# Kernel optimization log

Hardware: AMD Instinct MI355X
Metric: run time of the kernel (lower is better)

Reference implementation:

```python
import jax, jax.numpy as jnp
import numpy as np

B = 65536       # batch size
C = 100         # num classes (len(cls_num_list))
ALPHA = 0.01    # soft-label blend weight
TAU = 2.0       # init arg tau
TEMP = 2.0      # distillation temperature
EPS = 1e-9


def _soft_ce(logits, soft_targets):
    # -(soft * log softmax(logits)).sum(1).mean()
    return -(soft_targets * jax.nn.log_softmax(logits, axis=1)).sum(axis=1).mean()


def _inverse_prior(prior):
    idx0 = jnp.argsort(prior)            # ascending sort permutation
    value = prior[idx0]                  # sorted values
    idx1 = jnp.argsort(idx0)             # rank of each element
    idx2 = prior.shape[0] - 1 - idx1     # mirrored rank
    return value[idx2]


def setup_inputs():
    key = jax.random.key(0)
    ks = jax.random.split(key, 8)
    cls_num = np.arange(500, 0, -5).astype(np.float32)  # matches init cls_num_list
    prior = jnp.asarray(cls_num / cls_num.sum(), dtype=jnp.float32)
    return {
        "output_logits": jax.random.normal(ks[0], (B, C), jnp.float32),
        "target": jax.random.randint(ks[1], (B,), 0, C),
        "cos_feature": jax.random.normal(ks[2], (C, C), jnp.float32),
        "old_pred": jax.random.normal(ks[3], (B, C), jnp.float32),
        "expert1_logits": jax.random.normal(ks[4], (B, C), jnp.float32),
        "expert2_logits": jax.random.normal(ks[5], (B, C), jnp.float32),
        "expert3_logits": jax.random.normal(ks[6], (B, C), jnp.float32),
        "output": jax.random.normal(ks[7], (B, C), jnp.float32),
        "prior": prior,
        "epoch": 5,
    }


def reference(output_logits, target, cos_feature, old_pred, expert1_logits,
              expert2_logits, expert3_logits, output, prior, epoch):
    num_classes = prior.shape[0]
    # ---- convert_to_soft_labels (vectorized: gather rows of sim matrix, softmax, blend) ----
    one_hot = jax.nn.one_hot(target, num_classes, dtype=jnp.float32)          # [B,C]
    sim_probs = jax.nn.softmax(cos_feature, axis=1)[target]                   # [B,C]
    label = (1.0 - ALPHA) * one_hot + ALPHA * sim_probs

    # ---- three expert soft cross-entropies ----
    log_prior = jnp.log(prior + EPS)
    loss = _soft_ce(expert1_logits, label)
    loss = loss + _soft_ce(expert2_logits + log_prior, label)
    inv_prior = _inverse_prior(prior)
    loss = loss + _soft_ce(expert3_logits + log_prior - TAU * jnp.log(inv_prior + EPS), label)

    # ---- bincount-normalized summed logits ----
    counts = jnp.bincount(target, length=num_classes).astype(jnp.float32)     # [C]
    num = counts[target][:, None]                                             # [B,1]
    expert_sum_logits = output / num                                          # [B,C]

    # ---- masked KL distillation (only rows where teacher argmax == target) ----
    teacher_index = jnp.argmax(old_pred, axis=1)                              # argmax(softmax)=argmax
    mask = (teacher_index == target).astype(jnp.float32)                      # [B]
    t = jax.nn.softmax(old_pred / TEMP, axis=1)                               # teacher probs
    s = jax.nn.log_softmax(expert_sum_logits / TEMP, axis=1)                  # student log-probs
    log_t = jnp.where(t > 0, jnp.log(t), 0.0)
    kl_per = (t * (log_t - s)).sum(axis=1)                                    # [B] per-row KL
    n_sel = mask.sum()
    kl_loss = jnp.where(n_sel > 0, (kl_per * mask).sum() / jnp.maximum(n_sel, 1.0), 0.0)
    kl_loss = kl_loss * (TEMP ** 2) * 3.0

    return loss, kl_loss, expert_sum_logits
```

## Files before the change

### kernel.cpp

```cpp
#include <hip/hip_runtime.h>
#include <math.h>

#define B_N 65536
#define C_N 100
constexpr float ALPHA = 0.01f;
constexpr float TAU   = 2.0f;
constexpr float TEMP  = 2.0f;
constexpr float EPSF  = 1e-9f;
constexpr float NEG_SENT = -1.0e30f;

template<int CTRL>
__device__ __forceinline__ float fadd_dpp(float x) {
    return x + __int_as_float(__builtin_amdgcn_update_dpp(
        0, __float_as_int(x), CTRL, 0xF, 0xF, true));
}
__device__ __forceinline__ float rowsum32(float x) {
    x = fadd_dpp<0xB1>(x);
    x = fadd_dpp<0x4E>(x);
    x = fadd_dpp<0x124>(x);
    x = fadd_dpp<0x128>(x);
    x = fadd_dpp<0x142>(x);
    return x;
}
template<int CTRL>
__device__ __forceinline__ void amax_dpp(unsigned &hi, unsigned &lo) {
    const unsigned yh = (unsigned)__builtin_amdgcn_update_dpp(0, (int)hi, CTRL, 0xF, 0xF, true);
    const unsigned yl = (unsigned)__builtin_amdgcn_update_dpp(0, (int)lo, CTRL, 0xF, 0xF, true);
    const bool take = (yh > hi) || (yh == hi && yl > lo);
    hi = take ? yh : hi;
    lo = take ? yl : lo;
}
__device__ __forceinline__ void rowamax32(unsigned &hi, unsigned &lo) {
    amax_dpp<0xB1>(hi, lo);
    amax_dpp<0x4E>(hi, lo);
    amax_dpp<0x124>(hi, lo);
    amax_dpp<0x128>(hi, lo);
    amax_dpp<0x142>(hi, lo);
}

__device__ __forceinline__ float wsum(float v) {
    #pragma unroll
    for (int o = 32; o; o >>= 1) v += __shfl_xor(v, o);
    return v;
}

__global__ void prep_k(const float* __restrict__ cosf, const float* __restrict__ prior,
                       const int* __restrict__ target,
                       float* __restrict__ sm, float* __restrict__ w2,
                       float* __restrict__ w3, float* __restrict__ Ht,
                       int* __restrict__ counts) {
    const int b = blockIdx.x;
    if (b < 256) {
        __shared__ int h[C_N];
        for (int i = threadIdx.x; i < C_N; i += blockDim.x) h[i] = 0;
        __syncthreads();
        const int gid = b * blockDim.x + threadIdx.x;
        const int stride = 256 * blockDim.x;
        for (int i = gid; i < B_N; i += stride) atomicAdd(&h[target[i]], 1);
        __syncthreads();
        for (int i = threadIdx.x; i < C_N; i += blockDim.x)
            if (h[i]) atomicAdd(&counts[i], h[i]);
    } else if (b == 256) {
        __shared__ float sp[C_N];
        __shared__ float val[C_N];
        const int t = threadIdx.x;
        if (t < C_N) sp[t] = prior[t];
        __syncthreads();
        int rank = 0;
        float lpi = 0.f, pi = 0.f;
        if (t < C_N) {
            pi = sp[t];
            for (int j = 0; j < C_N; ++j) {
                const float pj = sp[j];
                rank += (pj < pi) || (pj == pi && j < t);
            }
            val[rank] = pi;
            lpi = __logf(pi + EPSF);
        }
        __syncthreads();
        if (t < C_N) {
            const float inv = val[C_N - 1 - rank];
            const float c3v = lpi - TAU * __logf(inv + EPSF);
            w2[t] = pi + EPSF;
            w3[t] = __expf(c3v);
            Ht[t] = lpi + c3v;
        }
    } else {
        const int gw = (b - 257) * 4 + (threadIdx.x >> 6);
        const int lane = threadIdx.x & 63;
        for (int row = gw; row < C_N; row += 16) {
            const float* rp = cosf + row * C_N;
            const float v0 = rp[lane];
            const bool has1 = (lane + 64) < C_N;
            const float v1 = has1 ? rp[lane + 64] : -INFINITY;
            float m = fmaxf(v0, v1);
            #pragma unroll
            for (int o = 32; o; o >>= 1) m = fmaxf(m, __shfl_xor(m, o));
            const float e0 = __expf(v0 - m);
            const float e1 = has1 ? __expf(v1 - m) : 0.f;
            const float s = wsum(e0 + e1);
            const float is = 1.0f / s;
            sm[row * C_N + lane] = e0 * is;
            if (has1) sm[row * C_N + lane + 64] = e1 * is;
        }
    }
}

#define HBLK 4096
#define NBLK (2 * HBLK)

__launch_bounds__(256)
__global__ void main_k(const int* __restrict__ target,
                       const float* __restrict__ e1p, const float* __restrict__ e2p,
                       const float* __restrict__ e3p, const float* __restrict__ opp,
                       const float* __restrict__ outp,
                       const float* __restrict__ sm, const float* __restrict__ w2p,
                       const float* __restrict__ w3p, const float* __restrict__ Hp,
                       const int* __restrict__ counts,
                       float* __restrict__ dout,
                       float* __restrict__ ploss, float* __restrict__ pkl, float* __restrict__ pn) {
    const int lane = threadIdx.x & 63;
    const int gl   = lane & 31;
    const int half = lane >> 5;
    const int wslot = threadIdx.x >> 6;
    const bool act = gl < 25;
    const int c0 = 4 * gl;
    const bool own = (gl == 16);
    __shared__ float bl[4], bk[4], bn[4];

    if (blockIdx.x < HBLK) {
        const int gw = blockIdx.x * 4 + wslot;
        const int rowA = 4 * gw + half;
        const int rowB = 4 * gw + 2 + half;
        const int tgtA = target[rowA];
        const int tgtB = target[rowB];
        const int baseA = rowA * C_N;
        const int baseB = rowB * C_N;

        float4 W2 = make_float4(0,0,0,0), W3 = make_float4(0,0,0,0), HH = make_float4(0,0,0,0);
        float4 E1A, E2A, E3A, E1B, E2B, E3B, SMA, SMB;
        E1A = E2A = E3A = E1B = E2B = E3B = make_float4(NEG_SENT, NEG_SENT, NEG_SENT, NEG_SENT);
        SMA = SMB = make_float4(0,0,0,0);
        if (act) {
            W2  = *(const float4*)(w2p + c0);
            W3  = *(const float4*)(w3p + c0);
            HH  = *(const float4*)(Hp + c0);
            E1A = *(const float4*)(e1p + baseA + c0);
            E1B = *(const float4*)(e1p + baseB + c0);
            E2A = *(const float4*)(e2p + baseA + c0);
            E2B = *(const float4*)(e2p + baseB + c0);
            E3A = *(const float4*)(e3p + baseA + c0);
            E3B = *(const float4*)(e3p + baseB + c0);
            SMA = *(const float4*)(sm + tgtA * C_N + c0);
            SMB = *(const float4*)(sm + tgtB * C_N + c0);
        }

        const float laA0 = (1.0f - ALPHA) * (c0     == tgtA) + ALPHA * SMA.x;
        const float laA1 = (1.0f - ALPHA) * (c0 + 1 == tgtA) + ALPHA * SMA.y;
        const float laA2 = (1.0f - ALPHA) * (c0 + 2 == tgtA) + ALPHA * SMA.z;
        const float laA3 = (1.0f - ALPHA) * (c0 + 3 == tgtA) + ALPHA * SMA.w;
        float s1A = __expf(E1A.x) + __expf(E1A.y) + __expf(E1A.z) + __expf(E1A.w);
        float s2A = W2.x * __expf(E2A.x) + W2.y * __expf(E2A.y)
                  + W2.z * __expf(E2A.z) + W2.w * __expf(E2A.w);
        float s3A = W3.x * __expf(E3A.x) + W3.y * __expf(E3A.y)
                  + W3.z * __expf(E3A.z) + W3.w * __expf(E3A.w);
        float dtA = laA0 * (E1A.x + E2A.x + E3A.x + HH.x)
                  + laA1 * (E1A.y + E2A.y + E3A.y + HH.y)
                  + laA2 * (E1A.z + E2A.z + E3A.z + HH.z)
                  + laA3 * (E1A.w + E2A.w + E3A.w + HH.w);
        const float laB0 = (1.0f - ALPHA) * (c0     == tgtB) + ALPHA * SMB.x;
        const float laB1 = (1.0f - ALPHA) * (c0 + 1 == tgtB) + ALPHA * SMB.y;
        const float laB2 = (1.0f - ALPHA) * (c0 + 2 == tgtB) + ALPHA * SMB.z;
        const float laB3 = (1.0f - ALPHA) * (c0 + 3 == tgtB) + ALPHA * SMB.w;
        float s1B = __expf(E1B.x) + __expf(E1B.y) + __expf(E1B.z) + __expf(E1B.w);
        float s2B = W2.x * __expf(E2B.x) + W2.y * __expf(E2B.y)
                  + W2.z * __expf(E2B.z) + W2.w * __expf(E2B.w);
        float s3B = W3.x * __expf(E3B.x) + W3.y * __expf(E3B.y)
                  + W3.z * __expf(E3B.z) + W3.w * __expf(E3B.w);
        float dtB = laB0 * (E1B.x + E2B.x + E3B.x + HH.x)
                  + laB1 * (E1B.y + E2B.y + E3B.y + HH.y)
                  + laB2 * (E1B.z + E2B.z + E3B.z + HH.z)
                  + laB3 * (E1B.w + E2B.w + E3B.w + HH.w);

        s1A = rowsum32(s1A);  s1B = rowsum32(s1B);
        s2A = rowsum32(s2A);  s2B = rowsum32(s2B);
        s3A = rowsum32(s3A);  s3B = rowsum32(s3B);
        dtA = rowsum32(dtA);  dtB = rowsum32(dtB);

        const float ceA = __logf(s1A * s2A * s3A) - dtA;
        const float ceB = __logf(s1B * s2B * s3B) - dtB;
        float lossAcc = own ? (ceA + ceB) : 0.f;
        const float lossW = __shfl(lossAcc, 16) + __shfl(lossAcc, 48);
        if (lane == 0) bl[wslot] = lossW;
        __syncthreads();
        if (threadIdx.x == 0)
            ploss[blockIdx.x] = bl[0] + bl[1] + bl[2] + bl[3];
    } else {
        const int j  = blockIdx.x - HBLK;
        const int gw = j * 4 + wslot;
        const int rowA = 4 * gw + half;
        const int rowB = 4 * gw + 2 + half;
        const int tgtA = target[rowA];
        const int tgtB = target[rowB];
        const int baseA = rowA * C_N;
        const int baseB = rowB * C_N;

        float4 OPA, OUA, OPB, OUB;
        OPA = OUA = OPB = OUB = make_float4(NEG_SENT, NEG_SENT, NEG_SENT, NEG_SENT);
        if (act) {
            OPA = *(const float4*)(opp + baseA + c0);
            OPB = *(const float4*)(opp + baseB + c0);
            OUA = *(const float4*)(outp + baseA + c0);
            OUB = *(const float4*)(outp + baseB + c0);
        }
        const float rcA = 1.0f / (float)counts[tgtA];
        const float rcB = 1.0f / (float)counts[tgtB];

        const float aA0 = OPA.x * 0.5f, aA1 = OPA.y * 0.5f, aA2 = OPA.z * 0.5f, aA3 = OPA.w * 0.5f;
        const float pA0 = __expf(aA0), pA1 = __expf(aA1), pA2 = __expf(aA2), pA3 = __expf(aA3);
        float ztA = pA0 + pA1 + pA2 + pA3;
        float bvA = OPA.x; int biA = c0;
        if (OPA.y > bvA) { bvA = OPA.y; biA = c0 + 1; }
        if (OPA.z > bvA) { bvA = OPA.z; biA = c0 + 2; }
        if (OPA.w > bvA) { bvA = OPA.w; biA = c0 + 3; }
        unsigned bbA = __float_as_uint(bvA);
        bbA = ((int)bbA < 0) ? ~bbA : (bbA | 0x80000000u);
        unsigned khiA = bbA, kloA = (unsigned)~biA;
        const float esA0 = OUA.x * rcA, esA1 = OUA.y * rcA, esA2 = OUA.z * rcA, esA3 = OUA.w * rcA;
        const float xA0 = esA0 * 0.5f, xA1 = esA1 * 0.5f, xA2 = esA2 * 0.5f, xA3 = esA3 * 0.5f;
        float zsA = __expf(xA0) + __expf(xA1) + __expf(xA2) + __expf(xA3);
        float DA  = pA0 * (aA0 - xA0) + pA1 * (aA1 - xA1) + pA2 * (aA2 - xA2) + pA3 * (aA3 - xA3);
        if (act) {
            *(float2*)(dout + 2 + baseA + c0)     = make_float2(esA0, esA1);
            *(float2*)(dout + 2 + baseA + c0 + 2) = make_float2(esA2, esA3);
        }
        const float aB0 = OPB.x * 0.5f, aB1 = OPB.y * 0.5f, aB2 = OPB.z * 0.5f, aB3 = OPB.w * 0.5f;
        const float pB0 = __expf(aB0), pB1 = __expf(aB1), pB2 = __expf(aB2), pB3 = __expf(aB3);
        float ztB = pB0 + pB1 + pB2 + pB3;
        float bvB = OPB.x; int biB = c0;
        if (OPB.y > bvB) { bvB = OPB.y; biB = c0 + 1; }
        if (OPB.z > bvB) { bvB = OPB.z; biB = c0 + 2; }
        if (OPB.w > bvB) { bvB = OPB.w; biB = c0 + 3; }
        unsigned bbB = __float_as_uint(bvB);
        bbB = ((int)bbB < 0) ? ~bbB : (bbB | 0x80000000u);
        unsigned khiB = bbB, kloB = (unsigned)~biB;
        const float esB0 = OUB.x * rcB, esB1 = OUB.y * rcB, esB2 = OUB.z * rcB, esB3 = OUB.w * rcB;
        const float xB0 = esB0 * 0.5f, xB1 = esB1 * 0.5f, xB2 = esB2 * 0.5f, xB3 = esB3 * 0.5f;
        float zsB = __expf(xB0) + __expf(xB1) + __expf(xB2) + __expf(xB3);
        float DB  = pB0 * (aB0 - xB0) + pB1 * (aB1 - xB1) + pB2 * (aB2 - xB2) + pB3 * (aB3 - xB3);
        if (act) {
            *(float2*)(dout + 2 + baseB + c0)     = make_float2(esB0, esB1);
            *(float2*)(dout + 2 + baseB + c0 + 2) = make_float2(esB2, esB3);
        }

        ztA = rowsum32(ztA);  ztB = rowsum32(ztB);
        zsA = rowsum32(zsA);  zsB = rowsum32(zsB);
        DA  = rowsum32(DA);   DB  = rowsum32(DB);
        rowamax32(khiA, kloA);
        rowamax32(khiB, kloB);

        const int miA = (int)~kloA;
        const int miB = (int)~kloB;
        const float rztA = 1.0f / ztA, rztB = 1.0f / ztB;
        const float klvA = DA * rztA + __logf(zsA * rztA);
        const float klvB = DB * rztB + __logf(zsB * rztB);
        const bool selA = own && (miA == tgtA);
        const bool selB = own && (miB == tgtB);
        float klAcc = (selA ? klvA : 0.f) + (selB ? klvB : 0.f);
        float nAcc  = (selA ? 1.f : 0.f) + (selB ? 1.f : 0.f);
        const float klW = __shfl(klAcc, 16) + __shfl(klAcc, 48);
        const float nW  = __shfl(nAcc, 16) + __shfl(nAcc, 48);
        if (lane == 0) { bk[wslot] = klW; bn[wslot] = nW; }
        __syncthreads();
        if (threadIdx.x == 0) {
            pkl[j] = bk[0] + bk[1] + bk[2] + bk[3];
            pn[j]  = bn[0] + bn[1] + bn[2] + bn[3];
        }
    }
}

__global__ void final_k(const float* __restrict__ ploss, const float* __restrict__ pkl,
                        const float* __restrict__ pn, float* __restrict__ dout) {
    __shared__ float sl[256], sk[256], sn[256];
    const int t = threadIdx.x;
    float l = 0.f, k = 0.f, n = 0.f;
    for (int i = t; i < HBLK; i += 256) { l += ploss[i]; k += pkl[i]; n += pn[i]; }
    sl[t] = l; sk[t] = k; sn[t] = n;
    __syncthreads();
    for (int s = 128; s; s >>= 1) {
        if (t < s) { sl[t] += sl[t + s]; sk[t] += sk[t + s]; sn[t] += sn[t + s]; }
        __syncthreads();
    }
    if (t == 0) {
        dout[0] = sl[0] / (float)B_N;
        const float kl = (sn[0] > 0.f) ? (sk[0] / fmaxf(sn[0], 1.f)) : 0.f;
        dout[1] = kl * (TEMP * TEMP) * 3.0f;
    }
}

extern "C" void kernel_launch(void* const* d_in, const int* in_sizes, int n_in,
                              void* d_out, int out_size, void* d_ws, size_t ws_size,
                              hipStream_t stream) {
    const int*   target = (const int*)  d_in[1];
    const float* cosf   = (const float*)d_in[2];
    const float* oldp   = (const float*)d_in[3];
    const float* e1     = (const float*)d_in[4];
    const float* e2     = (const float*)d_in[5];
    const float* e3     = (const float*)d_in[6];
    const float* outp   = (const float*)d_in[7];
    const float* prior  = (const float*)d_in[8];

    float* ws    = (float*)d_ws;
    float* sm    = ws;
    float* w2    = ws + 10016;
    float* w3    = ws + 10120;
    float* Ht    = ws + 10224;
    int*   cnts  = (int*)(ws + 10328);
    float* ploss = ws + 10432;
    float* pkl   = ploss + HBLK;
    float* pn    = pkl + HBLK;

    hipMemsetAsync(cnts, 0, C_N * sizeof(int), stream);
    prep_k<<<261, 256, 0, stream>>>(cosf, prior, target, sm, w2, w3, Ht, cnts);
    main_k<<<NBLK, 256, 0, stream>>>(target, e1, e2, e3, oldp, outp,
                                     sm, w2, w3, Ht, cnts, (float*)d_out, ploss, pkl, pn);
    final_k<<<1, 256, 0, stream>>>(ploss, pkl, pn, (float*)d_out);
}
```

Baseline: 51.79 us.

## Interleave block roles, use nontemporal output stores, and atomic bucketed partials

Even and odd blocks now alternate between the cross-entropy and KL roles, so both kinds of work run together across the GPU. The large normalized-logits output is written with nontemporal stores to avoid polluting cache. Per-block partials are accumulated into 256 buckets with float atomics, which shrinks the final reduction kernel. Occupancy is hinted via launch bounds. Float atomics make the summation order nondeterministic.

```diff
diff --git a/kernel.cpp b/kernel.cpp
--- a/kernel.cpp
+++ b/kernel.cpp
@@ -8,6 +8,8 @@
 constexpr float TEMP  = 2.0f;
 constexpr float EPSF  = 1e-9f;
 constexpr float NEG_SENT = -1.0e30f;
+
+typedef float v2f __attribute__((ext_vector_type(2)));
 
 template<int CTRL>
 __device__ __forceinline__ float fadd_dpp(float x) {
@@ -109,7 +111,7 @@
 #define HBLK 4096
 #define NBLK (2 * HBLK)
 
-__launch_bounds__(256)
+__launch_bounds__(256, 8)
 __global__ void main_k(const int* __restrict__ target,
                        const float* __restrict__ e1p, const float* __restrict__ e2p,
                        const float* __restrict__ e3p, const float* __restrict__ opp,
@@ -118,7 +120,7 @@
                        const float* __restrict__ w3p, const float* __restrict__ Hp,
                        const int* __restrict__ counts,
                        float* __restrict__ dout,
-                       float* __restrict__ ploss, float* __restrict__ pkl, float* __restrict__ pn) {
+                       float* __restrict__ pl, float* __restrict__ pk, float* __restrict__ pn) {
     const int lane = threadIdx.x & 63;
     const int gl   = lane & 31;
     const int half = lane >> 5;
@@ -127,9 +129,12 @@
     const int c0 = 4 * gl;
     const bool own = (gl == 16);
     __shared__ float bl[4], bk[4], bn[4];
-
-    if (blockIdx.x < HBLK) {
-        const int gw = blockIdx.x * 4 + wslot;
+    const int role = blockIdx.x & 1;
+    const int j    = blockIdx.x >> 1;
+    const int bucket = blockIdx.x & 255;
+
+    if (role == 0) {
+        const int gw = j * 4 + wslot;
         const int rowA = 4 * gw + half;
         const int rowB = 4 * gw + 2 + half;
         const int tgtA = target[rowA];
@@ -194,9 +199,8 @@
         if (lane == 0) bl[wslot] = lossW;
         __syncthreads();
         if (threadIdx.x == 0)
-            ploss[blockIdx.x] = bl[0] + bl[1] + bl[2] + bl[3];
+            atomicAdd(&pl[bucket], bl[0] + bl[1] + bl[2] + bl[3]);
     } else {
-        const int j  = blockIdx.x - HBLK;
         const int gw = j * 4 + wslot;
         const int rowA = 4 * gw + half;
         const int rowB = 4 * gw + 2 + half;
@@ -231,8 +235,10 @@
         float zsA = __expf(xA0) + __expf(xA1) + __expf(xA2) + __expf(xA3);
         float DA  = pA0 * (aA0 - xA0) + pA1 * (aA1 - xA1) + pA2 * (aA2 - xA2) + pA3 * (aA3 - xA3);
         if (act) {
-            *(float2*)(dout + 2 + baseA + c0)     = make_float2(esA0, esA1);
-            *(float2*)(dout + 2 + baseA + c0 + 2) = make_float2(esA2, esA3);
+            v2f w0 = { esA0, esA1 };
+            v2f w1 = { esA2, esA3 };
+            __builtin_nontemporal_store(w0, (v2f*)(dout + 2 + baseA + c0));
+            __builtin_nontemporal_store(w1, (v2f*)(dout + 2 + baseA + c0 + 2));
         }
         const float aB0 = OPB.x * 0.5f, aB1 = OPB.y * 0.5f, aB2 = OPB.z * 0.5f, aB3 = OPB.w * 0.5f;
         const float pB0 = __expf(aB0), pB1 = __expf(aB1), pB2 = __expf(aB2), pB3 = __expf(aB3);
@@ -249,8 +255,10 @@
         float zsB = __expf(xB0) + __expf(xB1) + __expf(xB2) + __expf(xB3);
         float DB  = pB0 * (aB0 - xB0) + pB1 * (aB1 - xB1) + pB2 * (aB2 - xB2) + pB3 * (aB3 - xB3);
         if (act) {
-            *(float2*)(dout + 2 + baseB + c0)     = make_float2(esB0, esB1);
-            *(float2*)(dout + 2 + baseB + c0 + 2) = make_float2(esB2, esB3);
+            v2f w0 = { esB0, esB1 };
+            v2f w1 = { esB2, esB3 };
+            __builtin_nontemporal_store(w0, (v2f*)(dout + 2 + baseB + c0));
+            __builtin_nontemporal_store(w1, (v2f*)(dout + 2 + baseB + c0 + 2));
         }
 
         ztA = rowsum32(ztA);  ztB = rowsum32(ztB);
@@ -273,19 +281,17 @@
         if (lane == 0) { bk[wslot] = klW; bn[wslot] = nW; }
         __syncthreads();
         if (threadIdx.x == 0) {
-            pkl[j] = bk[0] + bk[1] + bk[2] + bk[3];
-            pn[j]  = bn[0] + bn[1] + bn[2] + bn[3];
+            atomicAdd(&pk[bucket], bk[0] + bk[1] + bk[2] + bk[3]);
+            atomicAdd(&pn[bucket], bn[0] + bn[1] + bn[2] + bn[3]);
         }
     }
 }
 
-__global__ void final_k(const float* __restrict__ ploss, const float* __restrict__ pkl,
+__global__ void final_k(const float* __restrict__ pl, const float* __restrict__ pk,
                         const float* __restrict__ pn, float* __restrict__ dout) {
     __shared__ float sl[256], sk[256], sn[256];
     const int t = threadIdx.x;
-    float l = 0.f, k = 0.f, n = 0.f;
-    for (int i = t; i < HBLK; i += 256) { l += ploss[i]; k += pkl[i]; n += pn[i]; }
-    sl[t] = l; sk[t] = k; sn[t] = n;
+    sl[t] = pl[t]; sk[t] = pk[t]; sn[t] = pn[t];
     __syncthreads();
     for (int s = 128; s; s >>= 1) {
         if (t < s) { sl[t] += sl[t + s]; sk[t] += sk[t + s]; sn[t] += sn[t + s]; }
@@ -316,13 +322,13 @@
     float* w3    = ws + 10120;
     float* Ht    = ws + 10224;
     int*   cnts  = (int*)(ws + 10328);
-    float* ploss = ws + 10432;
-    float* pkl   = ploss + HBLK;
-    float* pn    = pkl + HBLK;
-
-    hipMemsetAsync(cnts, 0, C_N * sizeof(int), stream);
+    float* pl    = ws + 10432;
+    float* pk    = pl + 256;
+    float* pn    = pk + 256;
+
+    hipMemsetAsync(cnts, 0, (104 + 768) * sizeof(float), stream);
     prep_k<<<261, 256, 0, stream>>>(cosf, prior, target, sm, w2, w3, Ht, cnts);
     main_k<<<NBLK, 256, 0, stream>>>(target, e1, e2, e3, oldp, outp,
-                                     sm, w2, w3, Ht, cnts, (float*)d_out, ploss, pkl, pn);
-    final_k<<<1, 256, 0, stream>>>(ploss, pkl, pn, (float*)d_out);
-}
+                                     sm, w2, w3, Ht, cnts, (float*)d_out, pl, pk, pn);
+    final_k<<<1, 256, 0, stream>>>(pl, pk, pn, (float*)d_out);
+}
```

Result: faster. 46.77 us (-9.7%).
